# Kernel tuning notes

Measured on AMD Instinct MI355X. Metric: run time of the kernel, lower is better.

## Reference

```python
import jax, jax.numpy as jnp
import numpy as np

B, TMAX, C, H, NCLS = 256, 512, 128, 256, 400


def _lengths():
    rs = np.random.RandomState(0)
    lens = rs.randint(128, TMAX + 1, size=B)
    lens[0] = TMAX  # pin max length so T = TMAX
    return lens


def setup_inputs() -> dict:
    lens = _lengths()
    total = int(lens.sum())
    key = jax.random.key(0)
    ks = jax.random.split(key, 12)
    s_in, s_h = 1.0 / np.sqrt(C), 1.0 / np.sqrt(H)
    return {
        "input_features": jax.random.normal(ks[0], (total, C), jnp.float32),
        "segment_lengths": jnp.asarray(lens, jnp.int32),
        "W_ih": jax.random.normal(ks[1], (4 * H, C), jnp.float32) * s_h,
        "W_hh": jax.random.normal(ks[2], (4 * H, H), jnp.float32) * s_h,
        "b_ih": jax.random.normal(ks[3], (4 * H,), jnp.float32) * s_h,
        "b_hh": jax.random.normal(ks[4], (4 * H,), jnp.float32) * s_h,
        "h0_W1": jax.random.normal(ks[5], (C, C), jnp.float32) * s_in,
        "h0_W2": jax.random.normal(ks[6], (H, C), jnp.float32) * s_in,
        "c0_W1": jax.random.normal(ks[7], (C, C), jnp.float32) * s_in,
        "c0_W2": jax.random.normal(ks[8], (H, C), jnp.float32) * s_in,
        "fc_W": jax.random.normal(ks[9], (NCLS, H), jnp.float32) * s_h,
        "fc_b": jax.random.normal(ks[10], (NCLS,), jnp.float32) * s_h,
    }


def _lstm_step(x, h, c, W_ih, W_hh, b_ih, b_hh):
    # torch.nn.LSTMCell gate order: i, f, g, o
    gates = x @ W_ih.T + b_ih + h @ W_hh.T + b_hh
    i, f, g, o = jnp.split(gates, 4, axis=-1)
    c_new = jax.nn.sigmoid(f) * c + jax.nn.sigmoid(i) * jnp.tanh(g)
    h_new = jax.nn.sigmoid(o) * jnp.tanh(c_new)
    return h_new, c_new


def reference(input_features, segment_lengths, W_ih, W_hh, b_ih, b_hh,
              h0_W1, h0_W2, c0_W1, c0_W2, fc_W, fc_b):
    lens = np.asarray(segment_lengths)            # static ragged structure
    nb = lens.shape[0]
    T = int(lens.max())
    seg_id = np.repeat(np.arange(nb), lens)       # [total]
    offs = np.concatenate([np.arange(l) for l in lens])
    dt = input_features.dtype

    # pad_sequence(batch_first=True): [B, T, C]
    padded = jnp.zeros((nb, T, input_features.shape[1]), dt)
    padded = padded.at[jnp.asarray(seg_id), jnp.asarray(offs)].set(input_features)

    # 'input_means' in the original is actually a per-segment SUM
    sums = jax.ops.segment_sum(input_features, jnp.asarray(seg_id), num_segments=nb)
    h0 = jax.nn.relu(sums @ h0_W1.T) @ h0_W2.T
    c0 = jax.nn.relu(sums @ c0_W1.T) @ c0_W2.T

    def step(carry, x_t):
        h, c = carry
        h, c = _lstm_step(x_t, h, c, W_ih, W_hh, b_ih, b_hh)
        return (h, c), h

    xs = jnp.transpose(padded, (1, 0, 2))         # [T, B, C]
    _, h_outs = jax.lax.scan(step, (h0, c0), xs)  # [T, B, H]

    # Faithful to the original: h_outs is stacked time-first, yet indexed
    # h_outs[i, :segment_len] with i = batch index -> for segment i, mean over
    # the first min(len_i, B) BATCH rows of the hidden state at time t=i.
    lens_j = jnp.asarray(lens)
    mask = (jnp.arange(nb)[None, :] < lens_j[:, None]).astype(dt)   # [B(i), B(b)]
    count = jnp.minimum(lens_j, nb).astype(dt)                       # slice clamps at B
    fc_in = jnp.einsum('ib,ibh->ih', mask, h_outs[:nb]) / count[:, None]

    return fc_in @ fc_W.T + fc_b
```

## Files before the change

### kernel.cpp

```cpp
#include <hip/hip_runtime.h>
#include <hip/hip_bf16.h>
#include <stdint.h>

#define NB    256
#define CIN   128
#define HID   256
#define TST   256
#define NCLS  400

#define GRPS  16
#define MEMB  4
#define BPG   16
#define HPB   64
#define RPB   256
#define HXS   392
#define SPP   17

#define WS_SUMS   0u
#define WS_HEX    131072u
#define WS_C0     655360u
#define WS_CTRS   917504u
#define WS_PP     1048576u

typedef __attribute__((ext_vector_type(8))) short bf16x8;
typedef __attribute__((ext_vector_type(4))) float f32x4;
typedef unsigned long long u64;

__device__ __forceinline__ short f2bf(float f) {
  __hip_bfloat16 h = __float2bfloat16(f);
  return *reinterpret_cast<short*>(&h);
}
__device__ __forceinline__ float sigm(float v) { return 1.0f / (1.0f + __expf(-v)); }
__device__ __forceinline__ float tanh_(float v) {
  v = fminf(fmaxf(v, -15.0f), 15.0f);
  const float e = __expf(2.0f * v);
  return (e - 1.0f) / (e + 1.0f);
}

__global__ void k_segsum(const float* __restrict__ x, const int* __restrict__ lens,
                         float* __restrict__ sums) {
  const int b = blockIdx.x, t = threadIdx.x;
  __shared__ int   s_l[NB];
  __shared__ int   s_red[256];
  __shared__ float s_f[CIN];
  s_l[t] = lens[t];
  __syncthreads();
  int part = 0;
  for (int i = t; i < b; i += 256) part += s_l[i];
  s_red[t] = part; __syncthreads();
  for (int k = 128; k > 0; k >>= 1) { if (t < k) s_red[t] += s_red[t + k]; __syncthreads(); }
  const int off = s_red[0];
  const int len = s_l[b];
  const int c = t & 127, half = t >> 7;
  float a = 0.f;
  for (int r = half; r < len; r += 2) a += x[(size_t)(off + r) * CIN + c];
  if (half) s_f[c] = a;
  __syncthreads();
  if (!half) sums[b * CIN + c] = a + s_f[c];
}

__global__ void k_init(const float* __restrict__ sums,
                       const float* __restrict__ w1h, const float* __restrict__ w2h,
                       const float* __restrict__ w1c, const float* __restrict__ w2c,
                       u64* __restrict__ hexch, float* __restrict__ c0) {
  const int b = blockIdx.x, t = threadIdx.x;
  __shared__ float s_in[CIN], s_h[CIN], s_c[CIN];
  __shared__ __align__(8) short s_hb[HID];
  if (t < CIN) s_in[t] = sums[b * CIN + t];
  __syncthreads();
  {
    const int j = t & 127;
    const float* w = (t < CIN ? w1h : w1c) + j * CIN;
    float a = 0.f;
    #pragma unroll 8
    for (int k = 0; k < CIN; k++) a += s_in[k] * w[k];
    a = fmaxf(a, 0.f);
    if (t < CIN) s_h[j] = a; else s_c[j] = a;
  }
  __syncthreads();
  float ah = 0.f, ac = 0.f;
  const float* wh = w2h + t * CIN;
  const float* wc = w2c + t * CIN;
  #pragma unroll 8
  for (int k = 0; k < CIN; k++) { ah += s_h[k] * wh[k]; ac += s_c[k] * wc[k]; }
  s_hb[t] = f2bf(ah);
  c0[b * HID + t] = ac;
  __syncthreads();
  if (t < HID / 4)
    hexch[(size_t)b * 64 + t] = *(const u64*)&s_hb[t * 4];
}

__launch_bounds__(1024, 1)
__global__ void k_lstm(const float* __restrict__ x, const int* __restrict__ lens,
                       const float* __restrict__ Wih, const float* __restrict__ Whh,
                       const float* __restrict__ bih, const float* __restrict__ bhh,
                       const float* __restrict__ c0,
                       u64* __restrict__ hexch, float* __restrict__ pp,
                       int* __restrict__ ctrs) {
  const int p    = blockIdx.x;
  const int m    = p >> 4;
  const int grp  = p & 15;
  const int bat0 = grp * BPG;
  const int hid0 = m * HPB;

  const int t   = threadIdx.x;
  const int w   = t >> 6;
  const int kq  = w & 3;
  const int mq  = w >> 2;
  const int l15 = t & 15;
  const int hi  = (t >> 4) & 3;

  const int j2 = t & 63, b2 = t >> 6;
  const int ch = t & 127, bp2 = (t >> 7) * 2;

  __shared__ __align__(16) short s_hxb[BPG * HXS];
  __shared__ float s_part[4 * RPB * SPP];
  __shared__ float s_red[1024];
  __shared__ __align__(8) short s_hvalb[1024];
  __shared__ int   s_lens[NB];
  __shared__ int   s_off[BPG], s_len[BPG];

  if (t < NB) s_lens[t] = lens[t];
  __syncthreads();
  if (t < BPG) {
    int off = 0;
    for (int k = 0; k < bat0 + t; k++) off += s_lens[k];
    s_off[t] = off;
    s_len[t] = s_lens[bat0 + t];
  }
  __syncthreads();

  #define LOADA(AV, MT, KC) do {                                                   \
    const int lr_   = (MT) * 16 + l15;                                             \
    const int grow_ = (lr_ >> 6) * HID + hid0 + (lr_ & 63);                        \
    const int k0_   = kq * 96 + (KC) * 32 + hi * 8;                                \
    const float* src_ = (k0_ < CIN) ? (Wih + (size_t)grow_ * CIN + k0_)            \
                                    : (Whh + (size_t)grow_ * HID + (k0_ - CIN));   \
    const float4 f0_ = *(const float4*)(src_);                                     \
    const float4 f1_ = *(const float4*)(src_ + 4);                                 \
    AV[0]=f2bf(f0_.x); AV[1]=f2bf(f0_.y); AV[2]=f2bf(f0_.z); AV[3]=f2bf(f0_.w);    \
    AV[4]=f2bf(f1_.x); AV[5]=f2bf(f1_.y); AV[6]=f2bf(f1_.z); AV[7]=f2bf(f1_.w);    \
  } while (0)
  bf16x8 a00, a01, a02, a10, a11, a12, a20, a21, a22, a30, a31, a32;
  LOADA(a00, mq*4+0, 0); LOADA(a01, mq*4+0, 1); LOADA(a02, mq*4+0, 2);
  LOADA(a10, mq*4+1, 0); LOADA(a11, mq*4+1, 1); LOADA(a12, mq*4+1, 2);
  LOADA(a20, mq*4+2, 0); LOADA(a21, mq*4+2, 1); LOADA(a22, mq*4+2, 2);
  LOADA(a30, mq*4+3, 0); LOADA(a31, mq*4+3, 1); LOADA(a32, mq*4+3, 2);

  const float bias0 = bih[0*HID + hid0 + j2] + bhh[0*HID + hid0 + j2];
  const float bias1 = bih[1*HID + hid0 + j2] + bhh[1*HID + hid0 + j2];
  const float bias2 = bih[2*HID + hid0 + j2] + bhh[2*HID + hid0 + j2];
  const float bias3 = bih[3*HID + hid0 + j2] + bhh[3*HID + hid0 + j2];

  float c_reg = c0[(size_t)(bat0 + b2) * HID + hid0 + j2];

  float xp0, xp1;
  #define PREFX(S) do { \
    xp0 = ((S) < s_len[bp2+0]) ? x[(size_t)(s_off[bp2+0]+(S))*CIN+ch] : 0.f; \
    xp1 = ((S) < s_len[bp2+1]) ? x[(size_t)(s_off[bp2+1]+(S))*CIN+ch] : 0.f; \
  } while (0)
  #define STAGE(S) do { \
    s_hxb[(bp2+0)*HXS+ch] = f2bf(xp0); \
    s_hxb[(bp2+1)*HXS+ch] = f2bf(xp1); \
    const int b_ = t >> 6, q64_ = t & 63; \
    const u64 v_ = __hip_atomic_load( \
        hexch + ((size_t)((S) & 1) * NB + bat0 + b_) * 64 + q64_, \
        __ATOMIC_RELAXED, __HIP_MEMORY_SCOPE_AGENT); \
    *(u64*)&s_hxb[b_ * HXS + CIN + q64_ * 4] = v_; \
  } while (0)

  PREFX(0);
  STAGE(0);
  __syncthreads();

  for (int s = 0; s < TST; s++) {
    f32x4 d0 = {0.f,0.f,0.f,0.f}, d1 = {0.f,0.f,0.f,0.f};
    f32x4 d2 = {0.f,0.f,0.f,0.f}, d3 = {0.f,0.f,0.f,0.f};
    {
      const short* hxb = s_hxb + l15 * HXS + kq * 96 + hi * 8;
      bf16x8 bv;
      bv = *(const bf16x8*)(hxb + 0);
      d0 = __builtin_amdgcn_mfma_f32_16x16x32_bf16(a00, bv, d0, 0, 0, 0);
      d1 = __builtin_amdgcn_mfma_f32_16x16x32_bf16(a10, bv, d1, 0, 0, 0);
      d2 = __builtin_amdgcn_mfma_f32_16x16x32_bf16(a20, bv, d2, 0, 0, 0);
      d3 = __builtin_amdgcn_mfma_f32_16x16x32_bf16(a30, bv, d3, 0, 0, 0);
      bv = *(const bf16x8*)(hxb + 32);
      d0 = __builtin_amdgcn_mfma_f32_16x16x32_bf16(a01, bv, d0, 0, 0, 0);
      d1 = __builtin_amdgcn_mfma_f32_16x16x32_bf16(a11, bv, d1, 0, 0, 0);
      d2 = __builtin_amdgcn_mfma_f32_16x16x32_bf16(a21, bv, d2, 0, 0, 0);
      d3 = __builtin_amdgcn_mfma_f32_16x16x32_bf16(a31, bv, d3, 0, 0, 0);
      bv = *(const bf16x8*)(hxb + 64);
      d0 = __builtin_amdgcn_mfma_f32_16x16x32_bf16(a02, bv, d0, 0, 0, 0);
      d1 = __builtin_amdgcn_mfma_f32_16x16x32_bf16(a12, bv, d1, 0, 0, 0);
      d2 = __builtin_amdgcn_mfma_f32_16x16x32_bf16(a22, bv, d2, 0, 0, 0);
      d3 = __builtin_amdgcn_mfma_f32_16x16x32_bf16(a32, bv, d3, 0, 0, 0);
    }
    if (s < TST - 1) PREFX(s + 1);

    {
      float* spc = s_part + (size_t)(kq * RPB + mq * 64 + hi * 4) * SPP + l15;
      spc[(0*16 + 0)*SPP] = d0[0]; spc[(0*16 + 1)*SPP] = d0[1];
      spc[(0*16 + 2)*SPP] = d0[2]; spc[(0*16 + 3)*SPP] = d0[3];
      spc[(1*16 + 0)*SPP] = d1[0]; spc[(1*16 + 1)*SPP] = d1[1];
      spc[(1*16 + 2)*SPP] = d1[2]; spc[(1*16 + 3)*SPP] = d1[3];
      spc[(2*16 + 0)*SPP] = d2[0]; spc[(2*16 + 1)*SPP] = d2[1];
      spc[(2*16 + 2)*SPP] = d2[2]; spc[(2*16 + 3)*SPP] = d2[3];
      spc[(3*16 + 0)*SPP] = d3[0]; spc[(3*16 + 1)*SPP] = d3[1];
      spc[(3*16 + 2)*SPP] = d3[2]; spc[(3*16 + 3)*SPP] = d3[3];
    }
    __syncthreads();

    float g0 = bias0, g1 = bias1, g2 = bias2, g3 = bias3;
    #pragma unroll
    for (int q = 0; q < 4; q++) {
      const float* spq = s_part + (size_t)(q * RPB + j2) * SPP + b2;
      g0 += spq[(0 * 64) * SPP];
      g1 += spq[(1 * 64) * SPP];
      g2 += spq[(2 * 64) * SPP];
      g3 += spq[(3 * 64) * SPP];
    }
    c_reg = fmaf(sigm(g1), c_reg, sigm(g0) * tanh_(g2));
    const float h = sigm(g3) * tanh_(c_reg);

    s_hvalb[b2 * HPB + j2] = f2bf(h);
    s_red[b2 * HPB + j2]   = (bat0 + b2 < s_lens[s]) ? h : 0.f;
    __syncthreads();

    if (t < 256) {
      const int bb = t >> 4, qq = t & 15;
      const u64 v = *(const u64*)&s_hvalb[bb * HPB + qq * 4];
      __hip_atomic_store(
          hexch + ((size_t)((s + 1) & 1) * NB + bat0 + bb) * 64 + (hid0 >> 2) + qq,
          v, __ATOMIC_RELAXED, __HIP_MEMORY_SCOPE_AGENT);
    }
    if (t >= 512 && t < 512 + HPB) {
      const int jl = t - 512;
      float ps = 0.f;
      #pragma unroll
      for (int b = 0; b < BPG; b++) ps += s_red[b * HPB + jl];
      pp[(((size_t)s * GRPS + grp) * MEMB + m) * HPB + jl] = ps;
    }

    if (s == TST - 1) break;

    __syncthreads();

    if (t == 0) {
      __hip_atomic_fetch_add(ctrs + grp * 16, 1, __ATOMIC_RELAXED, __HIP_MEMORY_SCOPE_AGENT);
      const int target = MEMB * (s + 1);
      while (__hip_atomic_load(ctrs + grp * 16, __ATOMIC_RELAXED, __HIP_MEMORY_SCOPE_AGENT) < target)
        __builtin_amdgcn_s_sleep(1);
      asm volatile("" ::: "memory");
    }
    __syncthreads();
    STAGE(s + 1);
    __syncthreads();
  }
}

__global__ void k_out(const float* __restrict__ pp, const int* __restrict__ lens,
                      const float* __restrict__ fcW, const float* __restrict__ fcb,
                      float* __restrict__ out) {
  const int i = blockIdx.x, t = threadIdx.x;
  __shared__ float s_fc[HID];
  const int cnt = min(lens[i], NB);
  const int m = t >> 6, jl = t & 63;
  float a = 0.f;
  const float* base = pp + ((size_t)i * GRPS * MEMB + m) * HPB + jl;
  #pragma unroll 4
  for (int g = 0; g < GRPS; g++) a += base[(size_t)g * MEMB * HPB];
  s_fc[t] = a / (float)cnt;
  __syncthreads();
  for (int n = t; n < NCLS; n += 256) {
    float acc = fcb[n];
    const float4* w4 = (const float4*)(fcW + (size_t)n * HID);
    #pragma unroll 8
    for (int k4 = 0; k4 < HID / 4; k4++) {
      const float4 wv = w4[k4];
      acc = fmaf(s_fc[4*k4+0], wv.x, acc);
      acc = fmaf(s_fc[4*k4+1], wv.y, acc);
      acc = fmaf(s_fc[4*k4+2], wv.z, acc);
      acc = fmaf(s_fc[4*k4+3], wv.w, acc);
    }
    out[(size_t)i * NCLS + n] = acc;
  }
}

extern "C" void kernel_launch(void* const* d_in, const int* in_sizes, int n_in,
                              void* d_out, int out_size, void* d_ws, size_t ws_size,
                              hipStream_t stream) {
  const float* x    = (const float*)d_in[0];
  const int*   lens = (const int*)  d_in[1];
  const float* Wih  = (const float*)d_in[2];
  const float* Whh  = (const float*)d_in[3];
  const float* bih  = (const float*)d_in[4];
  const float* bhh  = (const float*)d_in[5];
  const float* w1h  = (const float*)d_in[6];
  const float* w2h  = (const float*)d_in[7];
  const float* w1c  = (const float*)d_in[8];
  const float* w2c  = (const float*)d_in[9];
  const float* fcW  = (const float*)d_in[10];
  const float* fcb  = (const float*)d_in[11];
  float* out = (float*)d_out;

  char* ws = (char*)d_ws;
  float* sums = (float*)(ws + WS_SUMS);
  u64*   hex  = (u64*)  (ws + WS_HEX);
  float* c0   = (float*)(ws + WS_C0);
  int*   ctrs = (int*)  (ws + WS_CTRS);
  float* pp   = (float*)(ws + WS_PP);

  hipMemsetAsync(ctrs, 0, GRPS * 16 * sizeof(int), stream);
  k_segsum<<<NB, 256, 0, stream>>>(x, lens, sums);
  k_init  <<<NB, 256, 0, stream>>>(sums, w1h, w2h, w1c, w2c, hex, c0);
  k_lstm  <<<GRPS * MEMB, 1024, 0, stream>>>(x, lens, Wih, Whh, bih, bhh, c0, hex, pp, ctrs);
  k_out   <<<NB, 256, 0, stream>>>(pp, lens, fcW, fcb, out);
}
```

Before: 877.3 us.

## Replace group barrier with per-member tags and local hidden-state reuse

Replaces the per-step group counter barrier, where thread 0 spins and the whole block then syncs, with per-member step tags in a double-buffered array. Each wave now waits only on the member block whose hidden slice it needs. A block's own hidden slice is copied directly from shared memory instead of being re-read from global. This removes one block-wide barrier and the serialized spin per step, at the cost of more spinning threads and relaxed-ordering visibility risks between the tag store and the data stores.

```diff
diff --git a/kernel.cpp b/kernel.cpp
--- a/kernel.cpp
+++ b/kernel.cpp
@@ -19,7 +19,7 @@
 #define WS_SUMS   0u
 #define WS_HEX    131072u
 #define WS_C0     655360u
-#define WS_CTRS   917504u
+#define WS_TAGS   917504u
 #define WS_PP     1048576u
 
 typedef __attribute__((ext_vector_type(8))) short bf16x8;
@@ -96,7 +96,7 @@
                        const float* __restrict__ bih, const float* __restrict__ bhh,
                        const float* __restrict__ c0,
                        u64* __restrict__ hexch, float* __restrict__ pp,
-                       int* __restrict__ ctrs) {
+                       int* __restrict__ tags) {
   const int p    = blockIdx.x;
   const int m    = p >> 4;
   const int grp  = p & 15;
@@ -163,10 +163,21 @@
     s_hxb[(bp2+0)*HXS+ch] = f2bf(xp0); \
     s_hxb[(bp2+1)*HXS+ch] = f2bf(xp1); \
     const int b_ = t >> 6, q64_ = t & 63; \
-    const u64 v_ = __hip_atomic_load( \
-        hexch + ((size_t)((S) & 1) * NB + bat0 + b_) * 64 + q64_, \
-        __ATOMIC_RELAXED, __HIP_MEMORY_SCOPE_AGENT); \
-    *(u64*)&s_hxb[b_ * HXS + CIN + q64_ * 4] = v_; \
+    const int mem_ = q64_ >> 4; \
+    if (mem_ == m && (S) > 0) { \
+      *(u64*)&s_hxb[b_ * HXS + CIN + q64_ * 4] = \
+          *(const u64*)&s_hvalb[b_ * HPB + (q64_ & 15) * 4]; \
+    } else { \
+      int* tg_ = tags + (((S) & 1) * GRPS + grp) * 16 + mem_ * 4; \
+      if (__hip_atomic_load(tg_, __ATOMIC_RELAXED, __HIP_MEMORY_SCOPE_AGENT) < (S)) { \
+        while (__hip_atomic_load(tg_, __ATOMIC_RELAXED, __HIP_MEMORY_SCOPE_AGENT) < (S)) \
+          __builtin_amdgcn_s_sleep(1); \
+      } \
+      const u64 v_ = __hip_atomic_load( \
+          hexch + ((size_t)((S) & 1) * NB + bat0 + b_) * 64 + q64_, \
+          __ATOMIC_RELAXED, __HIP_MEMORY_SCOPE_AGENT); \
+      *(u64*)&s_hxb[b_ * HXS + CIN + q64_ * 4] = v_; \
+    } \
   } while (0)
 
   PREFX(0);
@@ -245,14 +256,9 @@
 
     __syncthreads();
 
-    if (t == 0) {
-      __hip_atomic_fetch_add(ctrs + grp * 16, 1, __ATOMIC_RELAXED, __HIP_MEMORY_SCOPE_AGENT);
-      const int target = MEMB * (s + 1);
-      while (__hip_atomic_load(ctrs + grp * 16, __ATOMIC_RELAXED, __HIP_MEMORY_SCOPE_AGENT) < target)
-        __builtin_amdgcn_s_sleep(1);
-      asm volatile("" ::: "memory");
-    }
-    __syncthreads();
+    if (t == 0)
+      __hip_atomic_store(tags + (((s + 1) & 1) * GRPS + grp) * 16 + m * 4,
+                         s + 1, __ATOMIC_RELAXED, __HIP_MEMORY_SCOPE_AGENT);
     STAGE(s + 1);
     __syncthreads();
   }
@@ -307,12 +313,12 @@
   float* sums = (float*)(ws + WS_SUMS);
   u64*   hex  = (u64*)  (ws + WS_HEX);
   float* c0   = (float*)(ws + WS_C0);
-  int*   ctrs = (int*)  (ws + WS_CTRS);
+  int*   tags = (int*)  (ws + WS_TAGS);
   float* pp   = (float*)(ws + WS_PP);
 
-  hipMemsetAsync(ctrs, 0, GRPS * 16 * sizeof(int), stream);
+  hipMemsetAsync(tags, 0, 2 * GRPS * 16 * sizeof(int), stream);
   k_segsum<<<NB, 256, 0, stream>>>(x, lens, sums);
   k_init  <<<NB, 256, 0, stream>>>(sums, w1h, w2h, w1c, w2c, hex, c0);
-  k_lstm  <<<GRPS * MEMB, 1024, 0, stream>>>(x, lens, Wih, Whh, bih, bhh, c0, hex, pp, ctrs);
+  k_lstm  <<<GRPS * MEMB, 1024, 0, stream>>>(x, lens, Wih, Whh, bih, bhh, c0, hex, pp, tags);
   k_out   <<<NB, 256, 0, stream>>>(pp, lens, fcW, fcb, out);
 }
```

Result: faster. 853.5 us (-2.7%).
